# Optimization experiments

Hardware: AMD Instinct MI355X
Metric: run time of the kernel (lower is better)

## Reference

```python
import jax, jax.numpy as jnp
import numpy as np

INPUT_DIM, HIDDEN_DIM, OUTPUT_DIM = 64, 512, 64
BATCH, SEQ = 256, 512


def setup_inputs() -> dict:
    key = jax.random.key(0)
    ks = jax.random.split(key, 7)
    s_x = 1.0 / np.sqrt(INPUT_DIM)
    s_h = 1.0 / np.sqrt(HIDDEN_DIM)
    return {
        "x": jax.random.normal(ks[0], (BATCH, SEQ, INPUT_DIM), dtype=jnp.float32),
        "Wx": jax.random.uniform(ks[1], (HIDDEN_DIM, INPUT_DIM), minval=-s_x, maxval=s_x, dtype=jnp.float32),
        "bx": jax.random.uniform(ks[2], (HIDDEN_DIM,), minval=-s_x, maxval=s_x, dtype=jnp.float32),
        "Wh": jax.random.uniform(ks[3], (HIDDEN_DIM, HIDDEN_DIM), minval=-s_h, maxval=s_h, dtype=jnp.float32),
        "bh": jax.random.uniform(ks[4], (HIDDEN_DIM,), minval=-s_h, maxval=s_h, dtype=jnp.float32),
        "Wy": jax.random.uniform(ks[5], (OUTPUT_DIM, HIDDEN_DIM), minval=-s_h, maxval=s_h, dtype=jnp.float32),
        "by": jax.random.uniform(ks[6], (OUTPUT_DIM,), minval=-s_h, maxval=s_h, dtype=jnp.float32),
    }


def reference(x, Wx, bx, Wh, bh, Wy, by):
    # x: [B, T, I]. Precompute the input projection for all steps (one big GEMM),
    # then scan the sequential recurrence h_t = tanh(xproj_t + h_{t-1} @ Wh^T + bh).
    B = x.shape[0]
    xproj = jnp.einsum('bti,hi->bth', x, Wx) + bx  # [B, T, H]
    h0 = jnp.zeros((B, Wh.shape[0]), dtype=x.dtype)

    def step(h, xp_t):
        h = jnp.tanh(xp_t + h @ Wh.T + bh)
        return h, None

    hT, _ = jax.lax.scan(step, h0, jnp.swapaxes(xproj, 0, 1))  # scan over T
    y = hT @ Wy.T + by  # [B, O]
    return y
```

## Files before the change

### kernel.cpp

```cpp
#include <hip/hip_runtime.h>
#include <hip/hip_fp16.h>
#include <cstdint>
#include <cstddef>


constexpr int BATCH = 256;
constexpr int SEQ   = 512;
constexpr int IN    = 64;
constexpr int HID   = 512;
constexpr int OUT   = 64;
constexpr int T     = 1024;
constexpr int DTOT  = HID + IN;
constexpr int NS    = 4;
constexpr int DSL   = DTOT / NS;
constexpr int FR    = DSL / 8;
constexpr int NREG  = 27;
constexpr int NLDS  = 9;

typedef _Float16 half2v __attribute__((ext_vector_type(2)));

__device__ __forceinline__ float fdot2(uint32_t w, uint32_t h, float acc) {
    return __builtin_amdgcn_fdot2(__builtin_bit_cast(half2v, w),
                                  __builtin_bit_cast(half2v, h), acc, false);
}
__device__ __forceinline__ uint32_t packh2(float lo, float hi) {
    return (uint32_t)__half_as_ushort(__float2half(lo)) |
           ((uint32_t)__half_as_ushort(__float2half(hi)) << 16);
}
template <int CTRL>
__device__ __forceinline__ float dpp_add(float v) {
    int i = __builtin_bit_cast(int, v);
    int p = __builtin_amdgcn_update_dpp(i, i, CTRL, 0xF, 0xF, false);
    return v + __builtin_bit_cast(float, p);
}

__global__ __launch_bounds__(256, 1)
void prep_w(const float* __restrict__ Wh, const float* __restrict__ Wx,
            uint4* __restrict__ Wreg, uint4* __restrict__ Wlds) {
    const int idx = blockIdx.x * 256 + threadIdx.x;
    const int k = idx >> 10, t = idx & (T - 1);
    const int g = t >> 2, s = t & 3;
    const int o = (k < FR) ? 2 * g : 2 * g + 1;
    const int m = (k < FR) ? k : k - FR;
    const int j = DSL * s + 8 * m;
    const float* src = (j < HID) ? (Wh + (size_t)o * HID + j)
                                 : (Wx + (size_t)o * IN + (j - HID));
    uint4 d;
    d.x = packh2(src[0], src[1]);
    d.y = packh2(src[2], src[3]);
    d.z = packh2(src[4], src[5]);
    d.w = packh2(src[6], src[7]);
    if (k < NREG) Wreg[(size_t)k * T + t] = d;
    else          Wlds[(size_t)(k - NREG) * T + t] = d;
}

#define WREG_LIST(M) \
  M(0)  M(1)  M(2)  M(3)  M(4)  M(5)  M(6)  M(7)  M(8)  \
  M(9)  M(10) M(11) M(12) M(13) M(14) M(15) M(16) M(17) \
  M(18) M(19) M(20) M(21) M(22) M(23) M(24) M(25) M(26)

__global__ __launch_bounds__(T)
void rnn_main(const float* __restrict__ x,  const float* __restrict__ bx,
              const float* __restrict__ bh, const float* __restrict__ Wy,
              const float* __restrict__ by, const uint4* __restrict__ Wreg,
              const uint4* __restrict__ Wldg, float* __restrict__ y) {
    __shared__ uint4 wl[NLDS * T];
    __shared__ __align__(16) __half hb2[2][DTOT];

    const int b = blockIdx.x, t = threadIdx.x;
    const int g = t >> 2, s = t & 3;

    #pragma unroll
    for (int k = 0; k < NLDS; ++k) wl[k * T + t] = Wldg[(size_t)k * T + t];

#define DECL_W(n) uint4 w##n = Wreg[(size_t)(n) * T + t];
    WREG_LIST(DECL_W)
#undef DECL_W

    const float bb0 = bx[2 * g]     + bh[2 * g];
    const float bb1 = bx[2 * g + 1] + bh[2 * g + 1];
    const float* xb = x + (size_t)b * SEQ * IN;

    if (t < HID) hb2[0][t] = __float2half(0.0f);
    if (t < IN)  hb2[0][HID + t] = __float2half(xb[t]);
    float xv = (t < IN) ? xb[IN + t] : 0.0f;
    __syncthreads();

    for (int tt = 0; tt < SEQ; ++tt) {
        const int c = tt & 1;
        const uint4* hb = (const uint4*)(&hb2[c][DSL * s]);
        float a0 = 0.f, a1 = 0.f;

#define MACR(i, j) { const uint4 hv = hb[i];                          \
        a0 = fdot2(w##i.x, hv.x, a0); a0 = fdot2(w##i.y, hv.y, a0);   \
        a0 = fdot2(w##i.z, hv.z, a0); a0 = fdot2(w##i.w, hv.w, a0);   \
        a1 = fdot2(w##j.x, hv.x, a1); a1 = fdot2(w##j.y, hv.y, a1);   \
        a1 = fdot2(w##j.z, hv.z, a1); a1 = fdot2(w##j.w, hv.w, a1); }
        MACR(0,18) MACR(1,19) MACR(2,20) MACR(3,21) MACR(4,22)
        MACR(5,23) MACR(6,24) MACR(7,25) MACR(8,26)
#undef MACR
#define MACL(i, k) { const uint4 hv = hb[i];                          \
        const uint4 wv = wl[(k) * T + t];                             \
        a0 = fdot2(w##i.x, hv.x, a0); a0 = fdot2(w##i.y, hv.y, a0);   \
        a0 = fdot2(w##i.z, hv.z, a0); a0 = fdot2(w##i.w, hv.w, a0);   \
        a1 = fdot2(wv.x, hv.x, a1);   a1 = fdot2(wv.y, hv.y, a1);     \
        a1 = fdot2(wv.z, hv.z, a1);   a1 = fdot2(wv.w, hv.w, a1); }
        MACL(9,0)  MACL(10,1) MACL(11,2) MACL(12,3) MACL(13,4)
        MACL(14,5) MACL(15,6) MACL(16,7) MACL(17,8)
#undef MACL

        a0 = dpp_add<0xB1>(a0); a0 = dpp_add<0x4E>(a0);
        a1 = dpp_add<0xB1>(a1); a1 = dpp_add<0x4E>(a1);

        if (s == 0) {
            float z0 = a0 + bb0, z1 = a1 + bb1;
            z0 = fminf(fmaxf(z0, -15.f), 15.f);
            z1 = fminf(fmaxf(z1, -15.f), 15.f);
            const float e0 = __expf(2.f * z0), e1 = __expf(2.f * z1);
            const float h0 = 1.f - 2.f * __builtin_amdgcn_rcpf(e0 + 1.f);
            const float h1 = 1.f - 2.f * __builtin_amdgcn_rcpf(e1 + 1.f);
            ((uint32_t*)hb2[c ^ 1])[g] = packh2(h0, h1);
        }
        if (t < IN) {
            hb2[c ^ 1][HID + t] = __float2half(xv);
            if (tt + 2 < SEQ) xv = xb[(size_t)(tt + 2) * IN + t];
        }
        __syncthreads();
    }

    if (t < OUT) {
        float acc = by[t];
        const float* wy = Wy + (size_t)t * HID;
        #pragma unroll 8
        for (int j = 0; j < HID; ++j)
            acc = fmaf(wy[j], __half2float(hb2[0][j]), acc);
        y[(size_t)b * OUT + t] = acc;
    }
}

extern "C" void kernel_launch(void* const* d_in, const int* in_sizes, int n_in,
                              void* d_out, int out_size, void* d_ws, size_t ws_size,
                              hipStream_t stream) {
    const float* x  = (const float*)d_in[0];
    const float* Wx = (const float*)d_in[1];
    const float* bx = (const float*)d_in[2];
    const float* Wh = (const float*)d_in[3];
    const float* bh = (const float*)d_in[4];
    const float* Wy = (const float*)d_in[5];
    const float* by = (const float*)d_in[6];
    float* y = (float*)d_out;

    uint4* Wreg = (uint4*)d_ws;
    uint4* Wlds = Wreg + (size_t)NREG * T;

    hipLaunchKernelGGL(prep_w, dim3(36 * T / 256), dim3(256), 0, stream,
                       Wh, Wx, Wreg, Wlds);
    hipLaunchKernelGGL(rnn_main, dim3(BATCH), dim3(T), 0, stream,
                       x, bx, bh, Wy, by, Wreg, Wlds, y);
}
```

Before: 993.9 us.

## Halve block to 512 threads, four outputs per group, park weights in AGPRs

Each block now uses 512 threads, and each 4-thread group computes four hidden outputs instead of two. The weight slice per thread grows to 72 fragments: 21 are held in VGPRs, 32 are parked in accumulation registers through inline accvgpr writes and reads, and 19 sit in LDS. The goal is fewer threads per block, two blocks per CU, and more h-vector reuse per LDS load. The cost is extra accvgpr read instructions on the critical path, plus a risk of register spills or of LDS capacity limiting occupancy.

```diff
diff --git a/kernel.cpp b/kernel.cpp
--- a/kernel.cpp
+++ b/kernel.cpp
@@ -9,13 +9,11 @@
 constexpr int IN    = 64;
 constexpr int HID   = 512;
 constexpr int OUT   = 64;
-constexpr int T     = 1024;
+constexpr int T     = 512;
 constexpr int DTOT  = HID + IN;
-constexpr int NS    = 4;
-constexpr int DSL   = DTOT / NS;
-constexpr int FR    = DSL / 8;
-constexpr int NREG  = 27;
-constexpr int NLDS  = 9;
+constexpr int DSL   = DTOT / 4;
+constexpr int F_LDS0 = 53;
+constexpr int N_LDSF = 19;
 
 typedef _Float16 half2v __attribute__((ext_vector_type(2)));
 
@@ -36,13 +34,13 @@
 
 __global__ __launch_bounds__(256, 1)
 void prep_w(const float* __restrict__ Wh, const float* __restrict__ Wx,
-            uint4* __restrict__ Wreg, uint4* __restrict__ Wlds) {
+            uint4* __restrict__ Wpk) {
     const int idx = blockIdx.x * 256 + threadIdx.x;
-    const int k = idx >> 10, t = idx & (T - 1);
+    const int k = idx >> 9, t = idx & (T - 1);
+    const int p = k >> 2, r = k & 3;
     const int g = t >> 2, s = t & 3;
-    const int o = (k < FR) ? 2 * g : 2 * g + 1;
-    const int m = (k < FR) ? k : k - FR;
-    const int j = DSL * s + 8 * m;
+    const int o = 4 * g + r;
+    const int j = DSL * s + 8 * p;
     const float* src = (j < HID) ? (Wh + (size_t)o * HID + j)
                                  : (Wx + (size_t)o * IN + (j - HID));
     uint4 d;
@@ -50,76 +48,117 @@
     d.y = packh2(src[2], src[3]);
     d.z = packh2(src[4], src[5]);
     d.w = packh2(src[6], src[7]);
-    if (k < NREG) Wreg[(size_t)k * T + t] = d;
-    else          Wlds[(size_t)(k - NREG) * T + t] = d;
+    Wpk[idx] = d;
 }
 
-#define WREG_LIST(M) \
-  M(0)  M(1)  M(2)  M(3)  M(4)  M(5)  M(6)  M(7)  M(8)  \
-  M(9)  M(10) M(11) M(12) M(13) M(14) M(15) M(16) M(17) \
-  M(18) M(19) M(20) M(21) M(22) M(23) M(24) M(25) M(26)
+#define WV_LIST(M) \
+  M(0)  M(1)  M(2)  M(3)  M(4)  M(5)  M(6)  M(7)  M(8)  M(9)  M(10) \
+  M(11) M(12) M(13) M(14) M(15) M(16) M(17) M(18) M(19) M(20)
+#define AG_LIST(M) \
+  M(21) M(22) M(23) M(24) M(25) M(26) M(27) M(28) M(29) M(30) M(31) \
+  M(32) M(33) M(34) M(35) M(36) M(37) M(38) M(39) M(40) M(41) M(42) \
+  M(43) M(44) M(45) M(46) M(47) M(48) M(49) M(50) M(51) M(52)
 
-__global__ __launch_bounds__(T)
+#define MV(f, acc) { \
+    acc = fdot2(w##f.x, hv.x, acc); acc = fdot2(w##f.y, hv.y, acc); \
+    acc = fdot2(w##f.z, hv.z, acc); acc = fdot2(w##f.w, hv.w, acc); }
+#define MA(f, acc) { uint32_t q0, q1, q2, q3; \
+    asm volatile("v_accvgpr_read_b32 %0, %1" : "=v"(q0) : "a"(ag##f##_0)); \
+    asm volatile("v_accvgpr_read_b32 %0, %1" : "=v"(q1) : "a"(ag##f##_1)); \
+    asm volatile("v_accvgpr_read_b32 %0, %1" : "=v"(q2) : "a"(ag##f##_2)); \
+    asm volatile("v_accvgpr_read_b32 %0, %1" : "=v"(q3) : "a"(ag##f##_3)); \
+    acc = fdot2(q0, hv.x, acc); acc = fdot2(q1, hv.y, acc); \
+    acc = fdot2(q2, hv.z, acc); acc = fdot2(q3, hv.w, acc); }
+#define ML(f, acc) { const uint4 wv = wl[(size_t)((f) - F_LDS0) * T + t]; \
+    acc = fdot2(wv.x, hv.x, acc); acc = fdot2(wv.y, hv.y, acc); \
+    acc = fdot2(wv.z, hv.z, acc); acc = fdot2(wv.w, hv.w, acc); }
+
+__global__ __launch_bounds__(T, 2)
+__attribute__((amdgpu_waves_per_eu(2, 2)))
 void rnn_main(const float* __restrict__ x,  const float* __restrict__ bx,
               const float* __restrict__ bh, const float* __restrict__ Wy,
-              const float* __restrict__ by, const uint4* __restrict__ Wreg,
-              const uint4* __restrict__ Wldg, float* __restrict__ y) {
-    __shared__ uint4 wl[NLDS * T];
+              const float* __restrict__ by, const uint4* __restrict__ Wpk,
+              float* __restrict__ y) {
+    __shared__ uint4 wl[N_LDSF * T];
     __shared__ __align__(16) __half hb2[2][DTOT];
 
     const int b = blockIdx.x, t = threadIdx.x;
     const int g = t >> 2, s = t & 3;
 
     #pragma unroll
-    for (int k = 0; k < NLDS; ++k) wl[k * T + t] = Wldg[(size_t)k * T + t];
+    for (int i = 0; i < N_LDSF; ++i)
+        wl[i * T + t] = Wpk[(size_t)(F_LDS0 + i) * T + t];
 
-#define DECL_W(n) uint4 w##n = Wreg[(size_t)(n) * T + t];
-    WREG_LIST(DECL_W)
-#undef DECL_W
+#define DECL_WV(f) uint4 w##f = Wpk[(size_t)(f) * T + t];
+    WV_LIST(DECL_WV)
+#undef DECL_WV
 
-    const float bb0 = bx[2 * g]     + bh[2 * g];
-    const float bb1 = bx[2 * g + 1] + bh[2 * g + 1];
+#define DECL_AG(f) uint32_t ag##f##_0, ag##f##_1, ag##f##_2, ag##f##_3;
+    AG_LIST(DECL_AG)
+#undef DECL_AG
+#define LOAD_AG(f) { const uint4 tmp = Wpk[(size_t)(f) * T + t]; \
+    asm volatile("v_accvgpr_write_b32 %0, %1" : "=a"(ag##f##_0) : "v"(tmp.x)); \
+    asm volatile("v_accvgpr_write_b32 %0, %1" : "=a"(ag##f##_1) : "v"(tmp.y)); \
+    asm volatile("v_accvgpr_write_b32 %0, %1" : "=a"(ag##f##_2) : "v"(tmp.z)); \
+    asm volatile("v_accvgpr_write_b32 %0, %1" : "=a"(ag##f##_3) : "v"(tmp.w)); }
+    AG_LIST(LOAD_AG)
+#undef LOAD_AG
+
+    const float bb0 = bx[4 * g + 0] + bh[4 * g + 0];
+    const float bb1 = bx[4 * g + 1] + bh[4 * g + 1];
+    const float bb2 = bx[4 * g + 2] + bh[4 * g + 2];
+    const float bb3 = bx[4 * g + 3] + bh[4 * g + 3];
     const float* xb = x + (size_t)b * SEQ * IN;
 
-    if (t < HID) hb2[0][t] = __float2half(0.0f);
-    if (t < IN)  hb2[0][HID + t] = __float2half(xb[t]);
+    hb2[0][t] = __float2half(0.0f);
+    if (t < IN) hb2[0][HID + t] = __float2half(xb[t]);
     float xv = (t < IN) ? xb[IN + t] : 0.0f;
     __syncthreads();
 
+    #pragma unroll 1
     for (int tt = 0; tt < SEQ; ++tt) {
         const int c = tt & 1;
-        const uint4* hb = (const uint4*)(&hb2[c][DSL * s]);
-        float a0 = 0.f, a1 = 0.f;
+        const uint4* hbv =
+            (const uint4*)((const __half*)hb2[c] + DSL * s);
+        float a0 = 0.f, a1 = 0.f, a2 = 0.f, a3 = 0.f;
 
-#define MACR(i, j) { const uint4 hv = hb[i];                          \
-        a0 = fdot2(w##i.x, hv.x, a0); a0 = fdot2(w##i.y, hv.y, a0);   \
-        a0 = fdot2(w##i.z, hv.z, a0); a0 = fdot2(w##i.w, hv.w, a0);   \
-        a1 = fdot2(w##j.x, hv.x, a1); a1 = fdot2(w##j.y, hv.y, a1);   \
-        a1 = fdot2(w##j.z, hv.z, a1); a1 = fdot2(w##j.w, hv.w, a1); }
-        MACR(0,18) MACR(1,19) MACR(2,20) MACR(3,21) MACR(4,22)
-        MACR(5,23) MACR(6,24) MACR(7,25) MACR(8,26)
-#undef MACR
-#define MACL(i, k) { const uint4 hv = hb[i];                          \
-        const uint4 wv = wl[(k) * T + t];                             \
-        a0 = fdot2(w##i.x, hv.x, a0); a0 = fdot2(w##i.y, hv.y, a0);   \
-        a0 = fdot2(w##i.z, hv.z, a0); a0 = fdot2(w##i.w, hv.w, a0);   \
-        a1 = fdot2(wv.x, hv.x, a1);   a1 = fdot2(wv.y, hv.y, a1);     \
-        a1 = fdot2(wv.z, hv.z, a1);   a1 = fdot2(wv.w, hv.w, a1); }
-        MACL(9,0)  MACL(10,1) MACL(11,2) MACL(12,3) MACL(13,4)
-        MACL(14,5) MACL(15,6) MACL(16,7) MACL(17,8)
-#undef MACL
+        { const uint4 hv = hbv[0];  MV(0,a0)  MV(1,a1)  MV(2,a2)  MV(3,a3)  }
+        { const uint4 hv = hbv[1];  MV(4,a0)  MV(5,a1)  MV(6,a2)  MV(7,a3)  }
+        { const uint4 hv = hbv[2];  MV(8,a0)  MV(9,a1)  MV(10,a2) MV(11,a3) }
+        { const uint4 hv = hbv[3];  MV(12,a0) MV(13,a1) MV(14,a2) MV(15,a3) }
+        { const uint4 hv = hbv[4];  MV(16,a0) MV(17,a1) MV(18,a2) MV(19,a3) }
+        { const uint4 hv = hbv[5];  MV(20,a0) MA(21,a1) MA(22,a2) MA(23,a3) }
+        { const uint4 hv = hbv[6];  MA(24,a0) MA(25,a1) MA(26,a2) MA(27,a3) }
+        { const uint4 hv = hbv[7];  MA(28,a0) MA(29,a1) MA(30,a2) MA(31,a3) }
+        { const uint4 hv = hbv[8];  MA(32,a0) MA(33,a1) MA(34,a2) MA(35,a3) }
+        { const uint4 hv = hbv[9];  MA(36,a0) MA(37,a1) MA(38,a2) MA(39,a3) }
+        { const uint4 hv = hbv[10]; MA(40,a0) MA(41,a1) MA(42,a2) MA(43,a3) }
+        { const uint4 hv = hbv[11]; MA(44,a0) MA(45,a1) MA(46,a2) MA(47,a3) }
+        { const uint4 hv = hbv[12]; MA(48,a0) MA(49,a1) MA(50,a2) MA(51,a3) }
+        { const uint4 hv = hbv[13]; MA(52,a0) ML(53,a1) ML(54,a2) ML(55,a3) }
+        { const uint4 hv = hbv[14]; ML(56,a0) ML(57,a1) ML(58,a2) ML(59,a3) }
+        { const uint4 hv = hbv[15]; ML(60,a0) ML(61,a1) ML(62,a2) ML(63,a3) }
+        { const uint4 hv = hbv[16]; ML(64,a0) ML(65,a1) ML(66,a2) ML(67,a3) }
+        { const uint4 hv = hbv[17]; ML(68,a0) ML(69,a1) ML(70,a2) ML(71,a3) }
 
         a0 = dpp_add<0xB1>(a0); a0 = dpp_add<0x4E>(a0);
         a1 = dpp_add<0xB1>(a1); a1 = dpp_add<0x4E>(a1);
+        a2 = dpp_add<0xB1>(a2); a2 = dpp_add<0x4E>(a2);
+        a3 = dpp_add<0xB1>(a3); a3 = dpp_add<0x4E>(a3);
 
         if (s == 0) {
-            float z0 = a0 + bb0, z1 = a1 + bb1;
-            z0 = fminf(fmaxf(z0, -15.f), 15.f);
-            z1 = fminf(fmaxf(z1, -15.f), 15.f);
-            const float e0 = __expf(2.f * z0), e1 = __expf(2.f * z1);
-            const float h0 = 1.f - 2.f * __builtin_amdgcn_rcpf(e0 + 1.f);
-            const float h1 = 1.f - 2.f * __builtin_amdgcn_rcpf(e1 + 1.f);
-            ((uint32_t*)hb2[c ^ 1])[g] = packh2(h0, h1);
+            float z0 = fminf(fmaxf(a0 + bb0, -15.f), 15.f);
+            float z1 = fminf(fmaxf(a1 + bb1, -15.f), 15.f);
+            float z2 = fminf(fmaxf(a2 + bb2, -15.f), 15.f);
+            float z3 = fminf(fmaxf(a3 + bb3, -15.f), 15.f);
+            const float h0 = 1.f - 2.f * __builtin_amdgcn_rcpf(__expf(2.f * z0) + 1.f);
+            const float h1 = 1.f - 2.f * __builtin_amdgcn_rcpf(__expf(2.f * z1) + 1.f);
+            const float h2 = 1.f - 2.f * __builtin_amdgcn_rcpf(__expf(2.f * z2) + 1.f);
+            const float h3 = 1.f - 2.f * __builtin_amdgcn_rcpf(__expf(2.f * z3) + 1.f);
+            uint2 pk;
+            pk.x = packh2(h0, h1);
+            pk.y = packh2(h2, h3);
+            ((uint2*)hb2[c ^ 1])[g] = pk;
         }
         if (t < IN) {
             hb2[c ^ 1][HID + t] = __float2half(xv);
@@ -150,11 +189,10 @@
     const float* by = (const float*)d_in[6];
     float* y = (float*)d_out;
 
-    uint4* Wreg = (uint4*)d_ws;
-    uint4* Wlds = Wreg + (size_t)NREG * T;
+    uint4* Wpk = (uint4*)d_ws;
 
-    hipLaunchKernelGGL(prep_w, dim3(36 * T / 256), dim3(256), 0, stream,
-                       Wh, Wx, Wreg, Wlds);
+    hipLaunchKernelGGL(prep_w, dim3(72 * T / 256), dim3(256), 0, stream,
+                       Wh, Wx, Wpk);
     hipLaunchKernelGGL(rnn_main, dim3(BATCH), dim3(T), 0, stream,
-                       x, bx, bh, Wy, by, Wreg, Wlds, y);
+                       x, bx, bh, Wy, by, Wpk, y);
 }
```

Result: slower. 1.153 ms (+16.0%).

## Replace fdot2 recurrence with MFMA 16x16x32 f16 using register-resident weight fragments

Applied to the files above, without the earlier changes.

The per-step recurrence matvec moves from packed fdot2 with DPP reductions to MFMA 16x16x32 f16 instructions. Each wave keeps 36 weight A-fragments in registers, so the LDS-resident weight slice is no longer needed. Only one column of the B operand carries the hidden state; the other lanes read a zero buffer. Partial sums from the two K halves go through LDS with an extra barrier before the tanh. This spends most of the MFMA width on padding and adds a second sync per step, in exchange for fewer VALU instructions and no per-step LDS weight reads.

```diff
diff --git a/kernel.cpp b/kernel.cpp
--- a/kernel.cpp
+++ b/kernel.cpp
@@ -9,117 +9,113 @@
 constexpr int IN    = 64;
 constexpr int HID   = 512;
 constexpr int OUT   = 64;
-constexpr int T     = 1024;
+constexpr int TW    = 1024;
 constexpr int DTOT  = HID + IN;
-constexpr int NS    = 4;
-constexpr int DSL   = DTOT / NS;
-constexpr int FR    = DSL / 8;
-constexpr int NREG  = 27;
-constexpr int NLDS  = 9;
+constexpr int KHALF = 9;
+constexpr int NFRAG = 36;
 
-typedef _Float16 half2v __attribute__((ext_vector_type(2)));
+typedef _Float16 f16x8 __attribute__((ext_vector_type(8)));
+typedef float    f32x4 __attribute__((ext_vector_type(4)));
 
-__device__ __forceinline__ float fdot2(uint32_t w, uint32_t h, float acc) {
-    return __builtin_amdgcn_fdot2(__builtin_bit_cast(half2v, w),
-                                  __builtin_bit_cast(half2v, h), acc, false);
-}
 __device__ __forceinline__ uint32_t packh2(float lo, float hi) {
     return (uint32_t)__half_as_ushort(__float2half(lo)) |
            ((uint32_t)__half_as_ushort(__float2half(hi)) << 16);
 }
-template <int CTRL>
-__device__ __forceinline__ float dpp_add(float v) {
-    int i = __builtin_bit_cast(int, v);
-    int p = __builtin_amdgcn_update_dpp(i, i, CTRL, 0xF, 0xF, false);
-    return v + __builtin_bit_cast(float, p);
-}
 
 __global__ __launch_bounds__(256, 1)
 void prep_w(const float* __restrict__ Wh, const float* __restrict__ Wx,
-            uint4* __restrict__ Wreg, uint4* __restrict__ Wlds) {
+            uint4* __restrict__ Wpk) {
     const int idx = blockIdx.x * 256 + threadIdx.x;
-    const int k = idx >> 10, t = idx & (T - 1);
-    const int g = t >> 2, s = t & 3;
-    const int o = (k < FR) ? 2 * g : 2 * g + 1;
-    const int m = (k < FR) ? k : k - FR;
-    const int j = DSL * s + 8 * m;
-    const float* src = (j < HID) ? (Wh + (size_t)o * HID + j)
-                                 : (Wx + (size_t)o * IN + (j - HID));
+    const int l  = idx & 63;
+    const int wf = idx >> 6;
+    const int w  = wf / NFRAG;
+    const int f  = wf - w * NFRAG;
+    const int i  = f / KHALF;
+    const int kk = f - i * KHALF;
+    const int mg = w & 7, ph = w >> 3;
+    const int kt = ph * KHALF + kk;
+    const int o  = 64 * mg + 16 * i + (l & 15);
+    const int d0 = 32 * kt + 8 * (l >> 4);
+    const float* src = (d0 < HID) ? (Wh + (size_t)o * HID + d0)
+                                  : (Wx + (size_t)o * IN + (d0 - HID));
     uint4 d;
     d.x = packh2(src[0], src[1]);
     d.y = packh2(src[2], src[3]);
     d.z = packh2(src[4], src[5]);
     d.w = packh2(src[6], src[7]);
-    if (k < NREG) Wreg[(size_t)k * T + t] = d;
-    else          Wlds[(size_t)(k - NREG) * T + t] = d;
+    Wpk[idx] = d;
 }
 
-#define WREG_LIST(M) \
+#define FR_LIST(M) \
   M(0)  M(1)  M(2)  M(3)  M(4)  M(5)  M(6)  M(7)  M(8)  \
   M(9)  M(10) M(11) M(12) M(13) M(14) M(15) M(16) M(17) \
-  M(18) M(19) M(20) M(21) M(22) M(23) M(24) M(25) M(26)
+  M(18) M(19) M(20) M(21) M(22) M(23) M(24) M(25) M(26) \
+  M(27) M(28) M(29) M(30) M(31) M(32) M(33) M(34) M(35)
 
-__global__ __launch_bounds__(T)
+__global__ __launch_bounds__(TW)
+__attribute__((amdgpu_waves_per_eu(4, 4)))
 void rnn_main(const float* __restrict__ x,  const float* __restrict__ bx,
               const float* __restrict__ bh, const float* __restrict__ Wy,
-              const float* __restrict__ by, const uint4* __restrict__ Wreg,
-              const uint4* __restrict__ Wldg, float* __restrict__ y) {
-    __shared__ uint4 wl[NLDS * T];
+              const float* __restrict__ by, const uint4* __restrict__ Wpk,
+              float* __restrict__ y) {
     __shared__ __align__(16) __half hb2[2][DTOT];
+    __shared__ __align__(16) float  zb[2][HID];
+    __shared__ __align__(16) __half zsrc[8];
 
     const int b = blockIdx.x, t = threadIdx.x;
-    const int g = t >> 2, s = t & 3;
+    const int w = t >> 6, lane = t & 63;
+    const int mg = w & 7, ph = w >> 3;
+    const int g  = lane >> 4;
+    const bool real = (lane & 15) == 0;
 
-    #pragma unroll
-    for (int k = 0; k < NLDS; ++k) wl[k * T + t] = Wldg[(size_t)k * T + t];
-
-#define DECL_W(n) uint4 w##n = Wreg[(size_t)(n) * T + t];
-    WREG_LIST(DECL_W)
+    const uint4* wp = Wpk + (size_t)w * NFRAG * 64 + lane;
+#define DECL_W(f) const f16x8 w##f = __builtin_bit_cast(f16x8, wp[(f) * 64]);
+    FR_LIST(DECL_W)
 #undef DECL_W
 
-    const float bb0 = bx[2 * g]     + bh[2 * g];
-    const float bb1 = bx[2 * g + 1] + bh[2 * g + 1];
+    const float bs = (t < HID) ? bx[t] + bh[t] : 0.0f;
     const float* xb = x + (size_t)b * SEQ * IN;
 
     if (t < HID) hb2[0][t] = __float2half(0.0f);
     if (t < IN)  hb2[0][HID + t] = __float2half(xb[t]);
+    if (t < 8)   zsrc[t] = __float2half(0.0f);
     float xv = (t < IN) ? xb[IN + t] : 0.0f;
     __syncthreads();
 
+    const int bstep = real ? 4 : 0;
+
+    #pragma unroll 1
     for (int tt = 0; tt < SEQ; ++tt) {
         const int c = tt & 1;
-        const uint4* hb = (const uint4*)(&hb2[c][DSL * s]);
-        float a0 = 0.f, a1 = 0.f;
+        const uint4* bq = real ? ((const uint4*)&hb2[c][0]) + 36 * ph + g
+                               : (const uint4*)zsrc;
+        f32x4 a0 = {0.f,0.f,0.f,0.f}, a1 = {0.f,0.f,0.f,0.f};
+        f32x4 a2 = {0.f,0.f,0.f,0.f}, a3 = {0.f,0.f,0.f,0.f};
 
-#define MACR(i, j) { const uint4 hv = hb[i];                          \
-        a0 = fdot2(w##i.x, hv.x, a0); a0 = fdot2(w##i.y, hv.y, a0);   \
-        a0 = fdot2(w##i.z, hv.z, a0); a0 = fdot2(w##i.w, hv.w, a0);   \
-        a1 = fdot2(w##j.x, hv.x, a1); a1 = fdot2(w##j.y, hv.y, a1);   \
-        a1 = fdot2(w##j.z, hv.z, a1); a1 = fdot2(w##j.w, hv.w, a1); }
-        MACR(0,18) MACR(1,19) MACR(2,20) MACR(3,21) MACR(4,22)
-        MACR(5,23) MACR(6,24) MACR(7,25) MACR(8,26)
-#undef MACR
-#define MACL(i, k) { const uint4 hv = hb[i];                          \
-        const uint4 wv = wl[(k) * T + t];                             \
-        a0 = fdot2(w##i.x, hv.x, a0); a0 = fdot2(w##i.y, hv.y, a0);   \
-        a0 = fdot2(w##i.z, hv.z, a0); a0 = fdot2(w##i.w, hv.w, a0);   \
-        a1 = fdot2(wv.x, hv.x, a1);   a1 = fdot2(wv.y, hv.y, a1);     \
-        a1 = fdot2(wv.z, hv.z, a1);   a1 = fdot2(wv.w, hv.w, a1); }
-        MACL(9,0)  MACL(10,1) MACL(11,2) MACL(12,3) MACL(13,4)
-        MACL(14,5) MACL(15,6) MACL(16,7) MACL(17,8)
-#undef MACL
+#define KSTEP(fa, fb, fc, fd) { \
+        const f16x8 bfr = __builtin_bit_cast(f16x8, *bq); bq += bstep; \
+        a0 = __builtin_amdgcn_mfma_f32_16x16x32_f16(w##fa, bfr, a0, 0, 0, 0); \
+        a1 = __builtin_amdgcn_mfma_f32_16x16x32_f16(w##fb, bfr, a1, 0, 0, 0); \
+        a2 = __builtin_amdgcn_mfma_f32_16x16x32_f16(w##fc, bfr, a2, 0, 0, 0); \
+        a3 = __builtin_amdgcn_mfma_f32_16x16x32_f16(w##fd, bfr, a3, 0, 0, 0); }
+        KSTEP(0, 9, 18, 27)  KSTEP(1, 10, 19, 28)  KSTEP(2, 11, 20, 29)
+        KSTEP(3, 12, 21, 30) KSTEP(4, 13, 22, 31)  KSTEP(5, 14, 23, 32)
+        KSTEP(6, 15, 24, 33) KSTEP(7, 16, 25, 34)  KSTEP(8, 17, 26, 35)
+#undef KSTEP
 
-        a0 = dpp_add<0xB1>(a0); a0 = dpp_add<0x4E>(a0);
-        a1 = dpp_add<0xB1>(a1); a1 = dpp_add<0x4E>(a1);
+        if (real) {
+            f32x4* zp = (f32x4*)&zb[ph][64 * mg + 4 * g];
+            zp[0]  = a0;
+            zp[4]  = a1;
+            zp[8]  = a2;
+            zp[12] = a3;
+        }
+        __syncthreads();
 
-        if (s == 0) {
-            float z0 = a0 + bb0, z1 = a1 + bb1;
-            z0 = fminf(fmaxf(z0, -15.f), 15.f);
-            z1 = fminf(fmaxf(z1, -15.f), 15.f);
-            const float e0 = __expf(2.f * z0), e1 = __expf(2.f * z1);
-            const float h0 = 1.f - 2.f * __builtin_amdgcn_rcpf(e0 + 1.f);
-            const float h1 = 1.f - 2.f * __builtin_amdgcn_rcpf(e1 + 1.f);
-            ((uint32_t*)hb2[c ^ 1])[g] = packh2(h0, h1);
+        if (t < HID) {
+            const float z  = zb[0][t] + zb[1][t] + bs;
+            const float hh = 1.f - 2.f * __builtin_amdgcn_rcpf(__expf(2.f * z) + 1.f);
+            hb2[c ^ 1][t] = __float2half(hh);
         }
         if (t < IN) {
             hb2[c ^ 1][HID + t] = __float2half(xv);
@@ -150,11 +146,10 @@
     const float* by = (const float*)d_in[6];
     float* y = (float*)d_out;
 
-    uint4* Wreg = (uint4*)d_ws;
-    uint4* Wlds = Wreg + (size_t)NREG * T;
+    uint4* Wpk = (uint4*)d_ws;
 
-    hipLaunchKernelGGL(prep_w, dim3(36 * T / 256), dim3(256), 0, stream,
-                       Wh, Wx, Wreg, Wlds);
-    hipLaunchKernelGGL(rnn_main, dim3(BATCH), dim3(T), 0, stream,
-                       x, bx, bh, Wy, by, Wreg, Wlds, y);
+    hipLaunchKernelGGL(prep_w, dim3(16 * NFRAG * 64 / 256), dim3(256), 0, stream,
+                       Wh, Wx, Wpk);
+    hipLaunchKernelGGL(rnn_main, dim3(BATCH), dim3(TW), 0, stream,
+                       x, bx, bh, Wy, by, Wpk, y);
 }
```

After: 3.670 ms. 3.69x slower.
